# Kernel optimization log

Hardware: AMD Instinct MI355X
Metric: run time of the kernel (lower is better)

## Reference

```python
import jax, jax.numpy as jnp
import numpy as np

VOCAB = 49408
D = 768
H = 12
DH = D // H
FF = 3072
L = 4
B = 32
S = 512
EPS = 1e-6


def _pos_encoding(seq_len, d):
    pos = np.arange(seq_len, dtype=np.float64)[:, None]
    j = np.arange(d, dtype=np.float64)[None, :]
    ang = pos / np.power(10000.0, 2.0 * (j // 2) / d)
    pe = np.where((np.arange(d) % 2) == 0, np.sin(ang), np.cos(ang))
    return jnp.asarray(pe, dtype=jnp.float32)  # [seq_len, d]


def _layernorm(x, g, b):
    m = jnp.mean(x, axis=-1, keepdims=True)
    v = jnp.mean(jnp.square(x - m), axis=-1, keepdims=True)
    return g * (x - m) * jax.lax.rsqrt(v + EPS) + b


def setup_inputs() -> dict:
    key = jax.random.key(0)
    ks = jax.random.split(key, 16)
    s = 0.02
    inp = {
        "tokens": jax.random.randint(ks[0], (B, S), 0, VOCAB, dtype=jnp.int32),
        "emb": jax.random.normal(ks[1], (VOCAB, D), jnp.float32) * s,
        "wq": jax.random.normal(ks[2], (L, D, D), jnp.float32) * s,
        "bq": jnp.zeros((L, D), jnp.float32),
        "wk": jax.random.normal(ks[3], (L, D, D), jnp.float32) * s,
        "bk": jnp.zeros((L, D), jnp.float32),
        "wv": jax.random.normal(ks[4], (L, D, D), jnp.float32) * s,
        "bv": jnp.zeros((L, D), jnp.float32),
        "wo": jax.random.normal(ks[5], (L, D, D), jnp.float32) * s,
        "bo": jnp.zeros((L, D), jnp.float32),
        "w1": jax.random.normal(ks[6], (L, D, FF), jnp.float32) * s,
        "b1": jnp.zeros((L, FF), jnp.float32),
        "w2": jax.random.normal(ks[7], (L, FF, D), jnp.float32) * s,
        "b2": jnp.zeros((L, D), jnp.float32),
        "ln1_g": jnp.ones((L, D), jnp.float32),
        "ln1_b": jnp.zeros((L, D), jnp.float32),
        "ln2_g": jnp.ones((L, D), jnp.float32),
        "ln2_b": jnp.zeros((L, D), jnp.float32),
        "wl": jax.random.normal(ks[8], (D, 32), jnp.float32) * s,
        "bl": jnp.zeros((32,), jnp.float32),
        "wout": jax.random.normal(ks[9], (32, 1), jnp.float32) * s,
        "bout": jnp.zeros((1,), jnp.float32),
    }
    return inp


def reference(tokens, emb, wq, bq, wk, bk, wv, bv, wo, bo, w1, b1, w2, b2,
              ln1_g, ln1_b, ln2_g, ln2_b, wl, bl, wout, bout):
    seq_len = tokens.shape[1]
    pe = _pos_encoding(seq_len, D)  # [S, D] constant
    x = emb[tokens] * jnp.sqrt(jnp.float32(D)) + pe[None, :, :]  # [B,S,D]
    scale = 1.0 / jnp.sqrt(jnp.float32(DH))
    for i in range(L):
        # multi-head attention (naive full score matrix, mask=None)
        q = (jnp.einsum('bsd,de->bse', x, wq[i]) + bq[i]).reshape(-1, seq_len, H, DH)
        k = (jnp.einsum('bsd,de->bse', x, wk[i]) + bk[i]).reshape(-1, seq_len, H, DH)
        v = (jnp.einsum('bsd,de->bse', x, wv[i]) + bv[i]).reshape(-1, seq_len, H, DH)
        scores = jnp.einsum('bqhd,bkhd->bhqk', q, k) * scale  # [B,H,S,S]
        attn = jax.nn.softmax(scores, axis=-1)
        av = jnp.einsum('bhqk,bkhd->bqhd', attn, v).reshape(-1, seq_len, D)
        attn_out = jnp.einsum('bsd,de->bse', av, wo[i]) + bo[i]
        out1 = _layernorm(x + attn_out, ln1_g[i], ln1_b[i])
        # FFN: relu -> dense
        h = jax.nn.relu(jnp.einsum('bsd,df->bsf', out1, w1[i]) + b1[i])
        ffn = jnp.einsum('bsf,fd->bsd', h, w2[i]) + b2[i]
        x = _layernorm(out1 + ffn, ln2_g[i], ln2_b[i])
    pooled = jnp.mean(x, axis=1)  # GlobalAveragePooling1D -> [B,D]
    h = jax.nn.gelu(pooled @ wl + bl, approximate=False)
    out = jax.nn.sigmoid(h @ wout + bout)  # [B,1]
    return out
```

## Files before the change

### kernel.cpp

```cpp
#include <hip/hip_runtime.h>
#include <hip/hip_bf16.h>
#include <math.h>


#define B_  32
#define S_  512
#define D_  768
#define H_  12
#define DH_ 64
#define FF_ 3072
#define L_  4
#define QKVSTR 2304

typedef __attribute__((ext_vector_type(8))) short short8;
typedef __attribute__((ext_vector_type(4))) float f32x4;

__device__ __forceinline__ void async16(const void* g, void* l) {
    __builtin_amdgcn_global_load_lds(
        (const __attribute__((address_space(1))) void*)g,
        (__attribute__((address_space(3))) void*)l, 16, 0, 0);
}

__device__ __forceinline__ ushort f2bf(float f) {
    __hip_bfloat16 h = __float2bfloat16(f);
    return __builtin_bit_cast(ushort, h);
}

__device__ __forceinline__ short8 scale8_eighth(short8 v) {
    short8 r;
#pragma unroll
    for (int e = 0; e < 8; e++) {
        ushort u = (ushort)v[e];
        ushort ex = u & 0x7f80;
        r[e] = (short)(ex > 0x0180 ? (ushort)(u - 0x0180) : (ushort)(u & 0x8000));
    }
    return r;
}

__global__ void pe_kernel(float* __restrict__ pe) {
    int idx = blockIdx.x * 256 + threadIdx.x;
    if (idx >= S_ * D_) return;
    int s = idx / D_, j = idx % D_;
    double e = (2.0 * (double)(j >> 1)) / (double)D_;
    double denom = pow(10000.0, e);
    double ang = (double)s / denom;
    pe[idx] = (j & 1) ? (float)cos(ang) : (float)sin(ang);
}

__global__ void embed_kernel(const int* __restrict__ tokens,
                             const float* __restrict__ emb,
                             const float* __restrict__ pe,
                             float* __restrict__ x,
                             __hip_bfloat16* __restrict__ xb) {
    int row = blockIdx.x;
    int s = row & (S_ - 1);
    int tok = tokens[row];
    float scale = sqrtf((float)D_);
    for (int i = threadIdx.x; i < D_; i += 256) {
        float v = emb[(size_t)tok * D_ + i] * scale + pe[s * D_ + i];
        x[(size_t)row * D_ + i] = v;
        xb[(size_t)row * D_ + i] = __float2bfloat16(v);
    }
}

__global__ __launch_bounds__(256) void transpose_bf16_l(
    const float* __restrict__ in, __hip_bfloat16* __restrict__ out,
    int R, int C, size_t inL, size_t outL)
{
    __shared__ float tile[32][33];
    in  += (size_t)blockIdx.z * inL;
    out += (size_t)blockIdx.z * outL;
    int tx = threadIdx.x & 31, ty = threadIdx.x >> 5;
    int c0 = blockIdx.x * 32, r0 = blockIdx.y * 32;
#pragma unroll
    for (int d = 0; d < 32; d += 8)
        tile[ty + d][tx] = in[(size_t)(r0 + ty + d) * C + c0 + tx];
    __syncthreads();
#pragma unroll
    for (int d = 0; d < 32; d += 8)
        out[(size_t)(c0 + ty + d) * R + r0 + tx] = __float2bfloat16(tile[tx][ty + d]);
}

__global__ void biascat(const float* __restrict__ bq, const float* __restrict__ bk,
                        const float* __restrict__ bv, float* __restrict__ o) {
    int i = blockIdx.x * 256 + threadIdx.x;
    int ll = i / QKVSTR, j = i % QKVSTR;
    o[i] = j < 768 ? bq[ll * 768 + j]
         : j < 1536 ? bk[ll * 768 + j - 768]
                    : bv[ll * 768 + j - 1536];
}

#define BAR()   __builtin_amdgcn_s_barrier()
#define LGKM0() asm volatile("s_waitcnt lgkmcnt(0)" ::: "memory")
#define VM4()   asm volatile("s_waitcnt vmcnt(4)" ::: "memory")

#define STAGE_A(buf, h, kt) do { \
    async16(aSrc[h][0] + (kt) * 64, &lds[(buf) * 2][dOff[h][0]]); \
    async16(aSrc[h][1] + (kt) * 64, &lds[(buf) * 2][dOff[h][1]]); } while (0)
#define STAGE_B(buf, h, kt) do { \
    async16(bSrc[h][0] + (kt) * 64, &lds[(buf) * 2 + 1][dOff[h][0]]); \
    async16(bSrc[h][1] + (kt) * 64, &lds[(buf) * 2 + 1][dOff[h][1]]); } while (0)

#define LDA(buf, m, ks) (*(const short8*)((const char*)(&lds[(buf) * 2][0]) + \
    (size_t)((arow + (m) * 16) * 128 + cswz[ks])))
#define LDB(buf, n, ks) (*(const short8*)((const char*)(&lds[(buf) * 2 + 1][0]) + \
    (size_t)((brow + (n) * 16) * 128 + cswz[ks])))

#define MFMA_Q(mh, nh) do { \
    __builtin_amdgcn_s_setprio(1); \
    _Pragma("unroll") \
    for (int ks_ = 0; ks_ < 2; ks_++) { \
      _Pragma("unroll") \
      for (int n_ = 0; n_ < 2; n_++) { \
        _Pragma("unroll") \
        for (int m_ = 0; m_ < 4; m_++) { \
          acc[(mh) * 4 + m_][(nh) * 2 + n_] = \
              __builtin_amdgcn_mfma_f32_16x16x32_bf16( \
                  a[m_][ks_], b[(nh) * 2 + n_][ks_], \
                  acc[(mh) * 4 + m_][(nh) * 2 + n_], 0, 0, 0); \
        } } } \
    __builtin_amdgcn_s_setprio(0); \
} while (0)

template<int RELU>
__global__ __launch_bounds__(512, 2) void gemm256(
    const ushort* __restrict__ A,
    const ushort* __restrict__ Bt,
    const float* __restrict__ bias,
    __hip_bfloat16* __restrict__ C,
    int M, int N, int K, int NX)
{
    __shared__ alignas(16) ushort lds[4][16384];

    int t = threadIdx.x;
    int l = t & 63, w = t >> 6;
    int wmi = w >> 2, wni = w & 3;
    int lm = l & 15, lo = l >> 4;

    int nwg = gridDim.x;
    int bid = blockIdx.x;
    int lid = (nwg & 7) ? bid : ((bid & 7) * (nwg >> 3) + (bid >> 3));
    int bn = lid % NX, bm = lid / NX;
    int row0 = bm << 8, col0 = bn << 8;

    const ushort* aSrc[2][2];
    const ushort* bSrc[2][2];
    int dOff[2][2];
#pragma unroll
    for (int h = 0; h < 2; h++) {
#pragma unroll
        for (int c = 0; c < 2; c++) {
            int p = h * 16384 + c * 8192 + t * 16;
            int prow = p >> 7;
            int scolb = (p & 127) ^ ((prow & 7) << 4);
            dOff[h][c] = p >> 1;
            aSrc[h][c] = A  + (size_t)(row0 + prow) * K + (scolb >> 1);
            bSrc[h][c] = Bt + (size_t)(col0 + prow) * K + (scolb >> 1);
        }
    }

    int arow = wmi * 128 + lm;
    int brow = wni * 64 + lm;
    int swz = (lm & 7) << 4;
    int cswz[2];
    cswz[0] = (lo * 16) ^ swz;
    cswz[1] = (64 + lo * 16) ^ swz;

    f32x4 acc[8][4];
#pragma unroll
    for (int i = 0; i < 8; i++)
#pragma unroll
        for (int j = 0; j < 4; j++) acc[i][j] = (f32x4){0.f, 0.f, 0.f, 0.f};
    short8 a[4][2], b[4][2];

    const int NK = K >> 6;
    const int NI = NK >> 1;

    STAGE_A(0, 0, 0); STAGE_A(0, 1, 0);
    STAGE_B(0, 0, 0); STAGE_B(0, 1, 0);
    STAGE_B(1, 0, 1); STAGE_B(1, 1, 1);
    VM4();
    BAR();

    for (int i = 0; i < NI; i++) {
        int kt  = 2 * i;
        int ktA = (kt + 2 <= NK - 2) ? kt + 2 : NK - 2;
        int ktB = (kt + 3 <= NK - 1) ? kt + 3 : NK - 1;

#pragma unroll
        for (int m = 0; m < 4; m++) { a[m][0] = LDA(0, m, 0); a[m][1] = LDA(0, m, 1); }
#pragma unroll
        for (int n = 0; n < 2; n++) { b[n][0] = LDB(0, n, 0); b[n][1] = LDB(0, n, 1); }
        STAGE_A(1, 0, kt + 1);
        BAR(); LGKM0();
        MFMA_Q(0, 0);
        BAR();

#pragma unroll
        for (int n = 0; n < 2; n++) { b[2 + n][0] = LDB(0, 2 + n, 0); b[2 + n][1] = LDB(0, 2 + n, 1); }
        STAGE_A(1, 1, kt + 1);
        BAR(); LGKM0();
        MFMA_Q(0, 1);
        BAR();

#pragma unroll
        for (int m = 0; m < 4; m++) { a[m][0] = LDA(0, 4 + m, 0); a[m][1] = LDA(0, 4 + m, 1); }
        STAGE_B(0, 0, ktA);
        BAR(); LGKM0();
        MFMA_Q(1, 0);
        BAR();

        STAGE_B(0, 1, ktA);
        BAR(); LGKM0();
        MFMA_Q(1, 1);
        VM4();
        BAR();

#pragma unroll
        for (int m = 0; m < 4; m++) { a[m][0] = LDA(1, m, 0); a[m][1] = LDA(1, m, 1); }
#pragma unroll
        for (int n = 0; n < 2; n++) { b[n][0] = LDB(1, n, 0); b[n][1] = LDB(1, n, 1); }
        STAGE_A(0, 0, ktA);
        BAR(); LGKM0();
        MFMA_Q(0, 0);
        BAR();

#pragma unroll
        for (int n = 0; n < 2; n++) { b[2 + n][0] = LDB(1, 2 + n, 0); b[2 + n][1] = LDB(1, 2 + n, 1); }
        STAGE_A(0, 1, ktA);
        BAR(); LGKM0();
        MFMA_Q(0, 1);
        BAR();

#pragma unroll
        for (int m = 0; m < 4; m++) { a[m][0] = LDA(1, 4 + m, 0); a[m][1] = LDA(1, 4 + m, 1); }
        STAGE_B(1, 0, ktB);
        BAR(); LGKM0();
        MFMA_Q(1, 0);
        BAR();

        STAGE_B(1, 1, ktB);
        BAR(); LGKM0();
        MFMA_Q(1, 1);
        VM4();
        BAR();
    }

    int crow = row0 + wmi * 128;
    int ccol = col0 + wni * 64;
#pragma unroll
    for (int n = 0; n < 4; n++) {
        int c = ccol + n * 16 + lm;
        float bs = bias[c];
#pragma unroll
        for (int m = 0; m < 8; m++) {
#pragma unroll
            for (int r = 0; r < 4; r++) {
                float v = acc[m][n][r] + bs;
                if (RELU) v = fmaxf(v, 0.f);
                C[(size_t)(crow + m * 16 + lo * 4 + r) * N + c] = __float2bfloat16(v);
            }
        }
    }
    (void)M;
}

#define PSTR 72
__global__ __launch_bounds__(256) void attn_mfma(
    const ushort* __restrict__ qkv,
    __hip_bfloat16* __restrict__ av)
{
    __shared__ alignas(16) ushort sQP[128 * PSTR];
    __shared__ alignas(16) ushort sK[64 * PSTR];
    __shared__ alignas(16) ushort sVt[64 * PSTR];

    int t = threadIdx.x;
    int qt = blockIdx.x, h = blockIdx.y, b = blockIdx.z;
    int w = t >> 6, l = t & 63;
    int lm = l & 15, lq = l >> 4;
    int wm = w * 32;

    const ushort* qbase = qkv + (size_t)(b * S_ + qt * 128) * QKVSTR + h * DH_;
    const ushort* kbase = qkv + (size_t)b * S_ * QKVSTR + 768 + h * DH_;
    const ushort* vbase = qkv + (size_t)b * S_ * QKVSTR + 1536 + h * DH_;

    {
        int r = t >> 1, c0 = (t & 1) * 32;
        const ushort* src = qbase + (size_t)r * QKVSTR + c0;
        ushort* dst = &sQP[r * PSTR + c0];
        *(uint4*)(dst + 0)  = *(const uint4*)(src + 0);
        *(uint4*)(dst + 8)  = *(const uint4*)(src + 8);
        *(uint4*)(dst + 16) = *(const uint4*)(src + 16);
        *(uint4*)(dst + 24) = *(const uint4*)(src + 24);
    }
    __syncthreads();
    short8 qf[2][2];
#pragma unroll
    for (int i = 0; i < 2; i++)
#pragma unroll
        for (int ks = 0; ks < 2; ks++)
            qf[i][ks] = scale8_eighth(
                *(const short8*)&sQP[(wm + i * 16 + lm) * PSTR + ks * 32 + lq * 8]);

    ushort* sPw = &sQP[(size_t)wm * PSTR];

    f32x4 accO[2][4];
    float mrun[2][4], lrun[2][4];
#pragma unroll
    for (int i = 0; i < 2; i++)
#pragma unroll
        for (int j = 0; j < 4; j++) accO[i][j] = (f32x4){0.f, 0.f, 0.f, 0.f};
#pragma unroll
    for (int i = 0; i < 2; i++)
#pragma unroll
        for (int r = 0; r < 4; r++) { mrun[i][r] = -1e30f; lrun[i][r] = 0.f; }

    for (int kt = 0; kt < S_ / 64; kt++) {
        __syncthreads();
        {
            int r = t >> 2, c0 = (t & 3) * 16;
            const ushort* ksrc = kbase + (size_t)(kt * 64 + r) * QKVSTR + c0;
            ushort* kdst = &sK[r * PSTR + c0];
            *(uint4*)(kdst + 0) = *(const uint4*)(ksrc + 0);
            *(uint4*)(kdst + 8) = *(const uint4*)(ksrc + 8);
            const ushort* vsrc = vbase + (size_t)(kt * 64 + r) * QKVSTR + c0;
            ushort vv[16];
            *(uint4*)&vv[0] = *(const uint4*)(vsrc + 0);
            *(uint4*)&vv[8] = *(const uint4*)(vsrc + 8);
#pragma unroll
            for (int j = 0; j < 16; j++) sVt[(c0 + j) * PSTR + r] = vv[j];
        }
        __syncthreads();

        f32x4 accS[2][4];
#pragma unroll
        for (int i = 0; i < 2; i++)
#pragma unroll
            for (int j = 0; j < 4; j++) accS[i][j] = (f32x4){0.f, 0.f, 0.f, 0.f};
#pragma unroll
        for (int ks = 0; ks < 2; ks++) {
#pragma unroll
            for (int j = 0; j < 4; j++) {
                short8 kf = *(const short8*)&sK[(j * 16 + lm) * PSTR + ks * 32 + lq * 8];
#pragma unroll
                for (int i = 0; i < 2; i++)
                    accS[i][j] = __builtin_amdgcn_mfma_f32_16x16x32_bf16(
                        qf[i][ks], kf, accS[i][j], 0, 0, 0);
            }
        }

        float rmax[2][4];
#pragma unroll
        for (int i = 0; i < 2; i++)
#pragma unroll
            for (int r = 0; r < 4; r++)
                rmax[i][r] = fmaxf(fmaxf(accS[i][0][r], accS[i][1][r]),
                                   fmaxf(accS[i][2][r], accS[i][3][r]));
#pragma unroll
        for (int d = 1; d < 16; d <<= 1)
#pragma unroll
            for (int i = 0; i < 2; i++)
#pragma unroll
                for (int r = 0; r < 4; r++)
                    rmax[i][r] = fmaxf(rmax[i][r], __shfl_xor(rmax[i][r], d));

        float alpha[2][4];
#pragma unroll
        for (int i = 0; i < 2; i++)
#pragma unroll
            for (int r = 0; r < 4; r++) {
                float mn = fmaxf(mrun[i][r], rmax[i][r]);
                alpha[i][r] = __expf(mrun[i][r] - mn);
                mrun[i][r] = mn;
            }
        float rsum[2][4];
#pragma unroll
        for (int i = 0; i < 2; i++)
#pragma unroll
            for (int r = 0; r < 4; r++) rsum[i][r] = 0.f;
#pragma unroll
        for (int i = 0; i < 2; i++)
#pragma unroll
            for (int j = 0; j < 4; j++)
#pragma unroll
                for (int r = 0; r < 4; r++) {
                    float p = __expf(accS[i][j][r] - mrun[i][r]);
                    accS[i][j][r] = p;
                    rsum[i][r] += p;
                }
#pragma unroll
        for (int d = 1; d < 16; d <<= 1)
#pragma unroll
            for (int i = 0; i < 2; i++)
#pragma unroll
                for (int r = 0; r < 4; r++)
                    rsum[i][r] += __shfl_xor(rsum[i][r], d);
#pragma unroll
        for (int i = 0; i < 2; i++)
#pragma unroll
            for (int r = 0; r < 4; r++)
                lrun[i][r] = lrun[i][r] * alpha[i][r] + rsum[i][r];

#pragma unroll
        for (int i = 0; i < 2; i++)
#pragma unroll
            for (int j = 0; j < 4; j++)
#pragma unroll
                for (int r = 0; r < 4; r++) accO[i][j][r] *= alpha[i][r];

#pragma unroll
        for (int i = 0; i < 2; i++)
#pragma unroll
            for (int j = 0; j < 4; j++)
#pragma unroll
                for (int r = 0; r < 4; r++)
                    sPw[(i * 16 + lq * 4 + r) * PSTR + j * 16 + lm] =
                        f2bf(accS[i][j][r]);

#pragma unroll
        for (int ks = 0; ks < 2; ks++) {
            short8 pf[2];
#pragma unroll
            for (int i = 0; i < 2; i++)
                pf[i] = *(const short8*)&sPw[(i * 16 + lm) * PSTR + ks * 32 + lq * 8];
#pragma unroll
            for (int j = 0; j < 4; j++) {
                short8 vf = *(const short8*)&sVt[(j * 16 + lm) * PSTR + ks * 32 + lq * 8];
#pragma unroll
                for (int i = 0; i < 2; i++)
                    accO[i][j] = __builtin_amdgcn_mfma_f32_16x16x32_bf16(
                        pf[i], vf, accO[i][j], 0, 0, 0);
            }
        }
    }

    float invl[2][4];
#pragma unroll
    for (int i = 0; i < 2; i++)
#pragma unroll
        for (int r = 0; r < 4; r++) invl[i][r] = 1.0f / lrun[i][r];
#pragma unroll
    for (int i = 0; i < 2; i++)
#pragma unroll
        for (int j = 0; j < 4; j++)
#pragma unroll
            for (int r = 0; r < 4; r++) {
                int row = qt * 128 + wm + i * 16 + lq * 4 + r;
                int col = h * DH_ + j * 16 + lm;
                av[(size_t)(b * S_ + row) * D_ + col] =
                    __float2bfloat16(accO[i][j][r] * invl[i][r]);
            }
}

__global__ __launch_bounds__(256) void add_ln(float* __restrict__ x,
    __hip_bfloat16* __restrict__ xb,
    const __hip_bfloat16* __restrict__ r, const float* __restrict__ g,
    const float* __restrict__ bta)
{
    __shared__ float sred[256];
    int row = blockIdx.x, t = threadIdx.x;
    size_t base = (size_t)row * D_;
    float v0 = x[base + t]       + __bfloat162float(r[base + t]);
    float v1 = x[base + t + 256] + __bfloat162float(r[base + t + 256]);
    float v2 = x[base + t + 512] + __bfloat162float(r[base + t + 512]);
    sred[t] = v0 + v1 + v2;
    __syncthreads();
    for (int o = 128; o > 0; o >>= 1) { if (t < o) sred[t] += sred[t + o]; __syncthreads(); }
    float mean = sred[0] * (1.0f / D_);
    __syncthreads();
    float d0 = v0 - mean, d1 = v1 - mean, d2 = v2 - mean;
    sred[t] = d0 * d0 + d1 * d1 + d2 * d2;
    __syncthreads();
    for (int o = 128; o > 0; o >>= 1) { if (t < o) sred[t] += sred[t + o]; __syncthreads(); }
    float rstd = rsqrtf(sred[0] * (1.0f / D_) + 1e-6f);
    float o0 = g[t]       * d0 * rstd + bta[t];
    float o1 = g[t + 256] * d1 * rstd + bta[t + 256];
    float o2 = g[t + 512] * d2 * rstd + bta[t + 512];
    x[base + t]       = o0;
    x[base + t + 256] = o1;
    x[base + t + 512] = o2;
    xb[base + t]       = __float2bfloat16(o0);
    xb[base + t + 256] = __float2bfloat16(o1);
    xb[base + t + 512] = __float2bfloat16(o2);
}

__global__ void pool_kernel(const float* __restrict__ x, float* __restrict__ pooled) {
    int idx = blockIdx.x * 256 + threadIdx.x;
    int b = idx / D_, d = idx % D_;
    float acc = 0.f;
    const float* p = x + (size_t)b * S_ * D_ + d;
    for (int s = 0; s < S_; s++) acc += p[(size_t)s * D_];
    pooled[idx] = acc * (1.0f / S_);
}

__global__ void head_kernel(const float* __restrict__ pooled,
                            const float* __restrict__ wl,
                            const float* __restrict__ bl,
                            const float* __restrict__ wout,
                            const float* __restrict__ bout,
                            float* __restrict__ out)
{
    __shared__ float hb[32];
    int b = blockIdx.x, t = threadIdx.x;
    if (t < 32) {
        float z = bl[t];
        for (int d = 0; d < D_; d++) z += pooled[b * D_ + d] * wl[d * 32 + t];
        hb[t] = 0.5f * z * (1.0f + erff(z * 0.70710678118654752f));
    }
    __syncthreads();
    if (t == 0) {
        float z = bout[0];
        for (int j = 0; j < 32; j++) z += hb[j] * wout[j];
        out[b] = 1.0f / (1.0f + expf(-z));
    }
}

extern "C" void kernel_launch(void* const* d_in, const int* in_sizes, int n_in,
                              void* d_out, int out_size, void* d_ws, size_t ws_size,
                              hipStream_t stream)
{
    (void)in_sizes; (void)n_in; (void)out_size; (void)ws_size;
    const int*   tokens = (const int*)  d_in[0];
    const float* emb    = (const float*)d_in[1];
    const float* wq     = (const float*)d_in[2];
    const float* bq     = (const float*)d_in[3];
    const float* wk     = (const float*)d_in[4];
    const float* bk     = (const float*)d_in[5];
    const float* wv     = (const float*)d_in[6];
    const float* bv     = (const float*)d_in[7];
    const float* wo     = (const float*)d_in[8];
    const float* bo     = (const float*)d_in[9];
    const float* w1     = (const float*)d_in[10];
    const float* b1     = (const float*)d_in[11];
    const float* w2     = (const float*)d_in[12];
    const float* b2     = (const float*)d_in[13];
    const float* ln1g   = (const float*)d_in[14];
    const float* ln1b   = (const float*)d_in[15];
    const float* ln2g   = (const float*)d_in[16];
    const float* ln2b   = (const float*)d_in[17];
    const float* wl     = (const float*)d_in[18];
    const float* bl     = (const float*)d_in[19];
    const float* wout   = (const float*)d_in[20];
    const float* bout   = (const float*)d_in[21];
    float* out = (float*)d_out;

    char* ws = (char*)d_ws;
    size_t off = 0;
    auto alloc = [&](size_t n) -> void* {
        char* p = ws + off;
        off = (off + n + 255) & ~(size_t)255;
        return (void*)p;
    };
    const size_t XBYTES = (size_t)B_ * S_ * D_ * 4;
    const size_t XBF    = XBYTES / 2;
    float*          pe     = (float*)alloc((size_t)S_ * D_ * 4);
    float*          x      = (float*)alloc(XBYTES);
    __hip_bfloat16* xb     = (__hip_bfloat16*)alloc(XBF);
    __hip_bfloat16* r_bf   = (__hip_bfloat16*)alloc(XBF);
    char*           arena  = (char*)alloc(4 * XBF);
    __hip_bfloat16* qkv_bf = (__hip_bfloat16*)arena;
    __hip_bfloat16* av_bf  = (__hip_bfloat16*)(arena + 3 * XBF);
    __hip_bfloat16* h_bf   = (__hip_bfloat16*)arena;
    __hip_bfloat16* wT     = (__hip_bfloat16*)alloc((size_t)L_ * 7077888 * 2);
    float*          qkvbias= (float*)alloc((size_t)L_ * QKVSTR * 4);
    float*          pooled = (float*)alloc((size_t)B_ * D_ * 4);

    const int M = B_ * S_;
    const size_t DD = (size_t)D_ * D_;
    const size_t DF = (size_t)D_ * FF_;
    const size_t LSTRIDE = 4 * DD + 2 * DF;

    transpose_bf16_l<<<dim3(D_ / 32, D_ / 32, L_), 256, 0, stream>>>(
        wq, wT + 0 * DD, D_, D_, DD, LSTRIDE);
    transpose_bf16_l<<<dim3(D_ / 32, D_ / 32, L_), 256, 0, stream>>>(
        wk, wT + 1 * DD, D_, D_, DD, LSTRIDE);
    transpose_bf16_l<<<dim3(D_ / 32, D_ / 32, L_), 256, 0, stream>>>(
        wv, wT + 2 * DD, D_, D_, DD, LSTRIDE);
    transpose_bf16_l<<<dim3(D_ / 32, D_ / 32, L_), 256, 0, stream>>>(
        wo, wT + 3 * DD, D_, D_, DD, LSTRIDE);
    transpose_bf16_l<<<dim3(FF_ / 32, D_ / 32, L_), 256, 0, stream>>>(
        w1, wT + 4 * DD, D_, FF_, DF, LSTRIDE);
    transpose_bf16_l<<<dim3(D_ / 32, FF_ / 32, L_), 256, 0, stream>>>(
        w2, wT + 4 * DD + DF, FF_, D_, DF, LSTRIDE);
    biascat<<<(L_ * QKVSTR) / 256, 256, 0, stream>>>(bq, bk, bv, qkvbias);

    pe_kernel<<<(S_ * D_ + 255) / 256, 256, 0, stream>>>(pe);
    embed_kernel<<<M, 256, 0, stream>>>(tokens, emb, pe, x, xb);

    for (int l = 0; l < L_; l++) {
        __hip_bfloat16* wl_base = wT + (size_t)l * LSTRIDE;
        const ushort* qkvT = (const ushort*)(wl_base + 0 * DD);
        const ushort* woT  = (const ushort*)(wl_base + 3 * DD);
        const ushort* w1T  = (const ushort*)(wl_base + 4 * DD);
        const ushort* w2T  = (const ushort*)(wl_base + 4 * DD + DF);

        gemm256<0><<<dim3((QKVSTR / 256) * (M / 256)), 512, 0, stream>>>(
            (const ushort*)xb, qkvT, qkvbias + (size_t)l * QKVSTR, qkv_bf,
            M, QKVSTR, D_, QKVSTR / 256);

        attn_mfma<<<dim3(S_ / 128, H_, B_), 256, 0, stream>>>(
            (const ushort*)qkv_bf, av_bf);

        gemm256<0><<<dim3((D_ / 256) * (M / 256)), 512, 0, stream>>>(
            (const ushort*)av_bf, woT, bo + l * D_, r_bf, M, D_, D_, D_ / 256);
        add_ln<<<M, 256, 0, stream>>>(x, xb, r_bf, ln1g + l * D_, ln1b + l * D_);

        gemm256<1><<<dim3((FF_ / 256) * (M / 256)), 512, 0, stream>>>(
            (const ushort*)xb, w1T, b1 + l * FF_, h_bf, M, FF_, D_, FF_ / 256);
        gemm256<0><<<dim3((D_ / 256) * (M / 256)), 512, 0, stream>>>(
            (const ushort*)h_bf, w2T, b2 + l * D_, r_bf, M, D_, FF_, D_ / 256);
        add_ln<<<M, 256, 0, stream>>>(x, xb, r_bf, ln2g + l * D_, ln2b + l * D_);
    }

    pool_kernel<<<(B_ * D_) / 256, 256, 0, stream>>>(x, pooled);
    head_kernel<<<B_, 64, 0, stream>>>(pooled, wl, bl, wout, bout, out);
}
```

Before: 2.073 ms.

## Transpose attention MFMA operands so each lane owns a query row

Swaps the A/B operands of the QK^T and PV MFMAs so the accumulator is laid out with keys/head-dims along registers and queries along lanes. Each lane then holds one query row, which shrinks the softmax row max/sum reductions from four shuffle steps over eight values to two shuffles over two values, and allows vectorized short4 writes of P to LDS and of the output to global memory. The V transpose into LDS now packs two key rows per 32-bit store, replacing 16 scalar 16-bit stores. The cost is a different LDS access pattern, which could add bank conflicts.

```diff
diff --git a/kernel.cpp b/kernel.cpp
--- a/kernel.cpp
+++ b/kernel.cpp
@@ -13,6 +13,7 @@
 #define QKVSTR 2304
 
 typedef __attribute__((ext_vector_type(8))) short short8;
+typedef __attribute__((ext_vector_type(4))) short short4v;
 typedef __attribute__((ext_vector_type(4))) float f32x4;
 
 __device__ __forceinline__ void async16(const void* g, void* l) {
@@ -304,16 +305,14 @@
 
     ushort* sPw = &sQP[(size_t)wm * PSTR];
 
-    f32x4 accO[2][4];
-    float mrun[2][4], lrun[2][4];
-#pragma unroll
-    for (int i = 0; i < 2; i++)
-#pragma unroll
-        for (int j = 0; j < 4; j++) accO[i][j] = (f32x4){0.f, 0.f, 0.f, 0.f};
-#pragma unroll
-    for (int i = 0; i < 2; i++)
-#pragma unroll
-        for (int r = 0; r < 4; r++) { mrun[i][r] = -1e30f; lrun[i][r] = 0.f; }
+    f32x4 accO[4][2];
+    float mrun[2], lrun[2];
+#pragma unroll
+    for (int dk = 0; dk < 4; dk++)
+#pragma unroll
+        for (int i = 0; i < 2; i++) accO[dk][i] = (f32x4){0.f, 0.f, 0.f, 0.f};
+    mrun[0] = mrun[1] = -1e30f;
+    lrun[0] = lrun[1] = 0.f;
 
     for (int kt = 0; kt < S_ / 64; kt++) {
         __syncthreads();
@@ -323,99 +322,90 @@
             ushort* kdst = &sK[r * PSTR + c0];
             *(uint4*)(kdst + 0) = *(const uint4*)(ksrc + 0);
             *(uint4*)(kdst + 8) = *(const uint4*)(ksrc + 8);
-            const ushort* vsrc = vbase + (size_t)(kt * 64 + r) * QKVSTR + c0;
-            ushort vv[16];
-            *(uint4*)&vv[0] = *(const uint4*)(vsrc + 0);
-            *(uint4*)&vv[8] = *(const uint4*)(vsrc + 8);
-#pragma unroll
-            for (int j = 0; j < 16; j++) sVt[(c0 + j) * PSTR + r] = vv[j];
+            int p = t & 31, d0 = (t >> 5) * 8;
+            const ushort* vsrc = vbase + (size_t)(kt * 64 + 2 * p) * QKVSTR + d0;
+            uint4 v0 = *(const uint4*)(vsrc);
+            uint4 v1 = *(const uint4*)(vsrc + QKVSTR);
+            const ushort* e0 = (const ushort*)&v0;
+            const ushort* e1 = (const ushort*)&v1;
+#pragma unroll
+            for (int j = 0; j < 8; j++) {
+                uint pk = (uint)e0[j] | ((uint)e1[j] << 16);
+                *(uint*)&sVt[(d0 + j) * PSTR + 2 * p] = pk;
+            }
         }
         __syncthreads();
 
-        f32x4 accS[2][4];
+        f32x4 accS[4][2];
+#pragma unroll
+        for (int sb = 0; sb < 4; sb++)
+#pragma unroll
+            for (int i = 0; i < 2; i++) accS[sb][i] = (f32x4){0.f, 0.f, 0.f, 0.f};
+#pragma unroll
+        for (int ks = 0; ks < 2; ks++) {
+#pragma unroll
+            for (int sb = 0; sb < 4; sb++) {
+                short8 kf = *(const short8*)&sK[(sb * 16 + lm) * PSTR + ks * 32 + lq * 8];
+#pragma unroll
+                for (int i = 0; i < 2; i++)
+                    accS[sb][i] = __builtin_amdgcn_mfma_f32_16x16x32_bf16(
+                        kf, qf[i][ks], accS[sb][i], 0, 0, 0);
+            }
+        }
+
+        float pmax[2];
+#pragma unroll
+        for (int i = 0; i < 2; i++) {
+            float m0 = accS[0][i][0];
+#pragma unroll
+            for (int sb = 0; sb < 4; sb++)
+#pragma unroll
+                for (int r = 0; r < 4; r++) m0 = fmaxf(m0, accS[sb][i][r]);
+            m0 = fmaxf(m0, __shfl_xor(m0, 16));
+            m0 = fmaxf(m0, __shfl_xor(m0, 32));
+            pmax[i] = m0;
+        }
+        float alpha[2];
+#pragma unroll
+        for (int i = 0; i < 2; i++) {
+            float mn = fmaxf(mrun[i], pmax[i]);
+            alpha[i] = __expf(mrun[i] - mn);
+            mrun[i] = mn;
+        }
+        float rsum[2] = {0.f, 0.f};
+#pragma unroll
+        for (int sb = 0; sb < 4; sb++)
+#pragma unroll
+            for (int i = 0; i < 2; i++)
+#pragma unroll
+                for (int r = 0; r < 4; r++) {
+                    float p = __expf(accS[sb][i][r] - mrun[i]);
+                    accS[sb][i][r] = p;
+                    rsum[i] += p;
+                }
+#pragma unroll
+        for (int i = 0; i < 2; i++) {
+            rsum[i] += __shfl_xor(rsum[i], 16);
+            rsum[i] += __shfl_xor(rsum[i], 32);
+            lrun[i] = lrun[i] * alpha[i] + rsum[i];
+        }
+
+#pragma unroll
+        for (int dk = 0; dk < 4; dk++)
+#pragma unroll
+            for (int i = 0; i < 2; i++)
+#pragma unroll
+                for (int r = 0; r < 4; r++) accO[dk][i][r] *= alpha[i];
+
 #pragma unroll
         for (int i = 0; i < 2; i++)
 #pragma unroll
-            for (int j = 0; j < 4; j++) accS[i][j] = (f32x4){0.f, 0.f, 0.f, 0.f};
-#pragma unroll
-        for (int ks = 0; ks < 2; ks++) {
-#pragma unroll
-            for (int j = 0; j < 4; j++) {
-                short8 kf = *(const short8*)&sK[(j * 16 + lm) * PSTR + ks * 32 + lq * 8];
-#pragma unroll
-                for (int i = 0; i < 2; i++)
-                    accS[i][j] = __builtin_amdgcn_mfma_f32_16x16x32_bf16(
-                        qf[i][ks], kf, accS[i][j], 0, 0, 0);
+            for (int sb = 0; sb < 4; sb++) {
+                short4v pk;
+#pragma unroll
+                for (int r = 0; r < 4; r++) pk[r] = (short)f2bf(accS[sb][i][r]);
+                *(short4v*)&sPw[(i * 16 + lm) * PSTR + sb * 16 + lq * 4] = pk;
             }
-        }
-
-        float rmax[2][4];
-#pragma unroll
-        for (int i = 0; i < 2; i++)
-#pragma unroll
-            for (int r = 0; r < 4; r++)
-                rmax[i][r] = fmaxf(fmaxf(accS[i][0][r], accS[i][1][r]),
-                                   fmaxf(accS[i][2][r], accS[i][3][r]));
-#pragma unroll
-        for (int d = 1; d < 16; d <<= 1)
-#pragma unroll
-            for (int i = 0; i < 2; i++)
-#pragma unroll
-                for (int r = 0; r < 4; r++)
-                    rmax[i][r] = fmaxf(rmax[i][r], __shfl_xor(rmax[i][r], d));
-
-        float alpha[2][4];
-#pragma unroll
-        for (int i = 0; i < 2; i++)
-#pragma unroll
-            for (int r = 0; r < 4; r++) {
-                float mn = fmaxf(mrun[i][r], rmax[i][r]);
-                alpha[i][r] = __expf(mrun[i][r] - mn);
-                mrun[i][r] = mn;
-            }
-        float rsum[2][4];
-#pragma unroll
-        for (int i = 0; i < 2; i++)
-#pragma unroll
-            for (int r = 0; r < 4; r++) rsum[i][r] = 0.f;
-#pragma unroll
-        for (int i = 0; i < 2; i++)
-#pragma unroll
-            for (int j = 0; j < 4; j++)
-#pragma unroll
-                for (int r = 0; r < 4; r++) {
-                    float p = __expf(accS[i][j][r] - mrun[i][r]);
-                    accS[i][j][r] = p;
-                    rsum[i][r] += p;
-                }
-#pragma unroll
-        for (int d = 1; d < 16; d <<= 1)
-#pragma unroll
-            for (int i = 0; i < 2; i++)
-#pragma unroll
-                for (int r = 0; r < 4; r++)
-                    rsum[i][r] += __shfl_xor(rsum[i][r], d);
-#pragma unroll
-        for (int i = 0; i < 2; i++)
-#pragma unroll
-            for (int r = 0; r < 4; r++)
-                lrun[i][r] = lrun[i][r] * alpha[i][r] + rsum[i][r];
-
-#pragma unroll
-        for (int i = 0; i < 2; i++)
-#pragma unroll
-            for (int j = 0; j < 4; j++)
-#pragma unroll
-                for (int r = 0; r < 4; r++) accO[i][j][r] *= alpha[i][r];
-
-#pragma unroll
-        for (int i = 0; i < 2; i++)
-#pragma unroll
-            for (int j = 0; j < 4; j++)
-#pragma unroll
-                for (int r = 0; r < 4; r++)
-                    sPw[(i * 16 + lq * 4 + r) * PSTR + j * 16 + lm] =
-                        f2bf(accS[i][j][r]);
 
 #pragma unroll
         for (int ks = 0; ks < 2; ks++) {
@@ -424,32 +414,31 @@
             for (int i = 0; i < 2; i++)
                 pf[i] = *(const short8*)&sPw[(i * 16 + lm) * PSTR + ks * 32 + lq * 8];
 #pragma unroll
-            for (int j = 0; j < 4; j++) {
-                short8 vf = *(const short8*)&sVt[(j * 16 + lm) * PSTR + ks * 32 + lq * 8];
+            for (int dk = 0; dk < 4; dk++) {
+                short8 vf = *(const short8*)&sVt[(dk * 16 + lm) * PSTR + ks * 32 + lq * 8];
 #pragma unroll
                 for (int i = 0; i < 2; i++)
-                    accO[i][j] = __builtin_amdgcn_mfma_f32_16x16x32_bf16(
-                        pf[i], vf, accO[i][j], 0, 0, 0);
+                    accO[dk][i] = __builtin_amdgcn_mfma_f32_16x16x32_bf16(
+                        vf, pf[i], accO[dk][i], 0, 0, 0);
             }
         }
     }
 
-    float invl[2][4];
-#pragma unroll
-    for (int i = 0; i < 2; i++)
-#pragma unroll
-        for (int r = 0; r < 4; r++) invl[i][r] = 1.0f / lrun[i][r];
-#pragma unroll
-    for (int i = 0; i < 2; i++)
-#pragma unroll
-        for (int j = 0; j < 4; j++)
-#pragma unroll
-            for (int r = 0; r < 4; r++) {
-                int row = qt * 128 + wm + i * 16 + lq * 4 + r;
-                int col = h * DH_ + j * 16 + lm;
-                av[(size_t)(b * S_ + row) * D_ + col] =
-                    __float2bfloat16(accO[i][j][r] * invl[i][r]);
-            }
+    float invl[2];
+    invl[0] = 1.0f / lrun[0];
+    invl[1] = 1.0f / lrun[1];
+#pragma unroll
+    for (int i = 0; i < 2; i++) {
+        int row = qt * 128 + wm + i * 16 + lm;
+        __hip_bfloat16* dst = av + (size_t)(b * S_ + row) * D_ + h * DH_;
+#pragma unroll
+        for (int dk = 0; dk < 4; dk++) {
+            short4v ok;
+#pragma unroll
+            for (int r = 0; r < 4; r++) ok[r] = (short)f2bf(accO[dk][i][r] * invl[i]);
+            *(short4v*)(dst + dk * 16 + lq * 4) = ok;
+        }
+    }
 }
 
 __global__ __launch_bounds__(256) void add_ln(float* __restrict__ x,
```

Result: faster. 1.963 ms (-5.3%).
